# Kernel tuning notes

Hardware: AMD Instinct MI355X
Metric: run time of the kernel (lower is better)

## Reference

```python
import jax, jax.numpy as jnp
import numpy as np

SEASONP = 24
HORIZON = 12
F_WINDOW = 512
N_WINDOWS = 32768


def setup_inputs() -> dict:
    key = jax.random.key(0)
    k1, k2, k3, k4 = jax.random.split(key, 4)
    x = jax.random.uniform(k1, (N_WINDOWS, F_WINDOW), dtype=jnp.float32)
    y = jax.random.uniform(k2, (N_WINDOWS,), dtype=jnp.float32)
    init_L = jax.random.uniform(k3, (N_WINDOWS,), dtype=jnp.float32)
    init_b = jnp.zeros((N_WINDOWS,), dtype=jnp.float32)
    init_S = jax.random.uniform(k4, (N_WINDOWS, SEASONP), dtype=jnp.float32)
    return {
        "x": x,
        "y": y,
        "init_L": init_L,
        "init_b": init_b,
        "init_S": init_S,
        "alpha": jnp.float32(0.3),
        "beta": jnp.float32(0.1),
        "gamma": jnp.float32(0.2),
    }


def reference(x, y, init_L, init_b, init_S, alpha, beta, gamma):
    # Holt-Winters additive-seasonal recurrence, vectorized over N windows.
    # x: [N, F], init_L/init_b: [N], init_S: [N, P]
    N, F = x.shape
    P = init_S.shape[1]
    xt = x.T  # [F, N] time-major for scan
    idxs = jnp.arange(1, F, dtype=jnp.int32)

    def step(carry, inp):
        L, b, S = carry
        xi, i = inp
        si = i % P
        Sv = S[:, si]  # seasonal component for this phase, [N]
        Ln = alpha * (xi - Sv) + (1.0 - alpha) * (L + b)
        bn = beta * (Ln - L) + (1.0 - beta) * b
        Sn = S.at[:, si].set(gamma * (xi - Ln) + (1.0 - gamma) * Sv)
        return (Ln, bn, Sn), None

    (L, b, S), _ = jax.lax.scan(step, (init_L, init_b, init_S), (xt[1:], idxs))

    # forecast: f = (L[-1] + horizon * b[-1]) * S[(i + horizon) % P], i = F-1
    s_idx = (F - 1 + HORIZON) % P
    f = (L + HORIZON * b) * S[:, s_idx]
    loss = jnp.sum((f - y) ** 2)
    return loss
```

## Files before the change

### kernel.cpp

```cpp
#include <hip/hip_runtime.h>


#define F_WINDOW 512
#define SEASONP  24
#define HORIZON  12

#define HW_STEP(xi, si) do {                       \
    const float Sv  = S[si];                       \
    const float d   = (xi) - Sv;                   \
    const float ad  = alpha * d;         \
    const float s_  = L + b;                       \
    const float Ln  = fmaf(oma, s_, ad);           \
    const float abd = beta * ad;         \
    const float tb  = fmaf(omab, b, abd);          \
    const float bn  = fmaf(ab, -L, tb);            \
    const float e   = (xi) - Ln;                   \
    const float gs  = omg * Sv;                    \
    S[si] = fmaf(gamma, e, gs);                    \
    L = Ln; b = bn;                                \
} while (0)

#define HW_BLOCK24(v0, v1, v2, v3, v4, v5) do {                                  \
    HW_STEP(v0.x,  4); HW_STEP(v0.y,  5); HW_STEP(v0.z,  6); HW_STEP(v0.w,  7); \
    HW_STEP(v1.x,  8); HW_STEP(v1.y,  9); HW_STEP(v1.z, 10); HW_STEP(v1.w, 11); \
    HW_STEP(v2.x, 12); HW_STEP(v2.y, 13); HW_STEP(v2.z, 14); HW_STEP(v2.w, 15); \
    HW_STEP(v3.x, 16); HW_STEP(v3.y, 17); HW_STEP(v3.z, 18); HW_STEP(v3.w, 19); \
    HW_STEP(v4.x, 20); HW_STEP(v4.y, 21); HW_STEP(v4.z, 22); HW_STEP(v4.w, 23); \
    HW_STEP(v5.x,  0); HW_STEP(v5.y,  1); HW_STEP(v5.z,  2); HW_STEP(v5.w,  3); \
} while (0)

__global__ __launch_bounds__(64) void holtwinter_kernel(
    const float* __restrict__ x,
    const float* __restrict__ y,
    const float* __restrict__ init_L,
    const float* __restrict__ init_b,
    const float* __restrict__ init_S,
    const float* __restrict__ p_alpha,
    const float* __restrict__ p_beta,
    const float* __restrict__ p_gamma,
    float* __restrict__ out)
{
    const int n = blockIdx.x * 64 + threadIdx.x;

    const float alpha = p_alpha[0];
    const float beta  = p_beta[0];
    const float gamma = p_gamma[0];
    const float oma   = 1.0f - alpha;
    const float ab    = alpha * beta;
    const float omab  = 1.0f - ab;
    const float omg   = 1.0f - gamma;

    const float* __restrict__ xr = x + (size_t)n * F_WINDOW;

    float S[SEASONP];
    {
        const float4* iS4 = (const float4*)(init_S + (size_t)n * SEASONP);
        float4 s0 = iS4[0], s1 = iS4[1], s2 = iS4[2];
        float4 s3 = iS4[3], s4 = iS4[4], s5 = iS4[5];
        S[0]=s0.x;  S[1]=s0.y;  S[2]=s0.z;  S[3]=s0.w;
        S[4]=s1.x;  S[5]=s1.y;  S[6]=s1.z;  S[7]=s1.w;
        S[8]=s2.x;  S[9]=s2.y;  S[10]=s2.z; S[11]=s2.w;
        S[12]=s3.x; S[13]=s3.y; S[14]=s3.z; S[15]=s3.w;
        S[16]=s4.x; S[17]=s4.y; S[18]=s4.z; S[19]=s4.w;
        S[20]=s5.x; S[21]=s5.y; S[22]=s5.z; S[23]=s5.w;
    }

    float L = init_L[n];
    float b = init_b[n];

    {
        const float4 v = *(const float4*)(xr);
        HW_STEP(v.y, 1);
        HW_STEP(v.z, 2);
        HW_STEP(v.w, 3);
    }

    float4 c0, c1, c2, c3, c4, c5;
    {
        const float* __restrict__ xp = xr + 4;
        c0 = *(const float4*)(xp +  0);
        c1 = *(const float4*)(xp +  4);
        c2 = *(const float4*)(xp +  8);
        c3 = *(const float4*)(xp + 12);
        c4 = *(const float4*)(xp + 16);
        c5 = *(const float4*)(xp + 20);
    }
    #pragma unroll 2
    for (int blk = 0; blk < 20; ++blk) {
        const float* __restrict__ np = xr + 4 + (blk + 1) * 24;
        const float4 n0 = *(const float4*)(np +  0);
        const float4 n1 = *(const float4*)(np +  4);
        const float4 n2 = *(const float4*)(np +  8);
        const float4 n3 = *(const float4*)(np + 12);
        const float4 n4 = *(const float4*)(np + 16);
        const float4 n5 = *(const float4*)(np + 20);

        HW_BLOCK24(c0, c1, c2, c3, c4, c5);

        c0 = n0; c1 = n1; c2 = n2; c3 = n3; c4 = n4; c5 = n5;
    }
    HW_BLOCK24(c0, c1, c2, c3, c4, c5);

    {
        const float4 v = *(const float4*)(xr + 508);
        HW_STEP(v.x, 4); HW_STEP(v.y, 5); HW_STEP(v.z, 6); HW_STEP(v.w, 7);
    }

    const float f    = fmaf((float)HORIZON, b, L) * S[19];
    const float diff = f - y[n];
    float val = diff * diff;

    #pragma unroll
    for (int off = 32; off > 0; off >>= 1)
        val += __shfl_down(val, off);
    if (threadIdx.x == 0)
        atomicAdd(out, val);
}

extern "C" void kernel_launch(void* const* d_in, const int* in_sizes, int n_in,
                              void* d_out, int out_size, void* d_ws, size_t ws_size,
                              hipStream_t stream) {
    const float* x      = (const float*)d_in[0];
    const float* y      = (const float*)d_in[1];
    const float* init_L = (const float*)d_in[2];
    const float* init_b = (const float*)d_in[3];
    const float* init_S = (const float*)d_in[4];
    const float* alpha  = (const float*)d_in[5];
    const float* beta   = (const float*)d_in[6];
    const float* gamma  = (const float*)d_in[7];
    float* out = (float*)d_out;

    const int N = in_sizes[1];

    hipMemsetAsync(d_out, 0, sizeof(float), stream);
    holtwinter_kernel<<<N / 64, 64, 0, stream>>>(
        x, y, init_L, init_b, init_S, alpha, beta, gamma, out);
}
```

Measured before the change: 118.7 us.

## Stage x through double-buffered LDS with coalesced cooperative loads

Each thread previously read its own 512-float row with strided float4 loads, so every wavefront load touched 64 separate rows. The new code has the 64-thread block cooperatively load 96-column super-blocks of all 64 rows with coalesced float4 loads into a padded LDS tile (stride 97). The tile is double-buffered so the next super-block's global loads overlap the recurrence on the current one. The final 28 steps still read directly from global memory. This adds about 50 KB of LDS per block, which can limit occupancy, plus scalar LDS reads inside the serial recurrence and 24 float4 staging registers.

```diff
diff --git a/kernel.cpp b/kernel.cpp
--- a/kernel.cpp
+++ b/kernel.cpp
@@ -4,6 +4,9 @@
 #define F_WINDOW 512
 #define SEASONP  24
 #define HORIZON  12
+#define ROWS     64
+#define LSTRIDE  97
+#define SB_F4    24
 
 #define HW_STEP(xi, si) do {                       \
     const float Sv  = S[si];                       \
@@ -20,6 +23,17 @@
     L = Ln; b = bn;                                \
 } while (0)
 
+#define HW_LDS24(row, B) do {                                                                \
+    HW_STEP((row)[(B)+ 0], 4); HW_STEP((row)[(B)+ 1], 5); HW_STEP((row)[(B)+ 2], 6);        \
+    HW_STEP((row)[(B)+ 3], 7); HW_STEP((row)[(B)+ 4], 8); HW_STEP((row)[(B)+ 5], 9);        \
+    HW_STEP((row)[(B)+ 6],10); HW_STEP((row)[(B)+ 7],11); HW_STEP((row)[(B)+ 8],12);        \
+    HW_STEP((row)[(B)+ 9],13); HW_STEP((row)[(B)+10],14); HW_STEP((row)[(B)+11],15);        \
+    HW_STEP((row)[(B)+12],16); HW_STEP((row)[(B)+13],17); HW_STEP((row)[(B)+14],18);        \
+    HW_STEP((row)[(B)+15],19); HW_STEP((row)[(B)+16],20); HW_STEP((row)[(B)+17],21);        \
+    HW_STEP((row)[(B)+18],22); HW_STEP((row)[(B)+19],23); HW_STEP((row)[(B)+20], 0);        \
+    HW_STEP((row)[(B)+21], 1); HW_STEP((row)[(B)+22], 2); HW_STEP((row)[(B)+23], 3);        \
+} while (0)
+
 #define HW_BLOCK24(v0, v1, v2, v3, v4, v5) do {                                  \
     HW_STEP(v0.x,  4); HW_STEP(v0.y,  5); HW_STEP(v0.z,  6); HW_STEP(v0.w,  7); \
     HW_STEP(v1.x,  8); HW_STEP(v1.y,  9); HW_STEP(v1.z, 10); HW_STEP(v1.w, 11); \
@@ -27,6 +41,22 @@
     HW_STEP(v3.x, 16); HW_STEP(v3.y, 17); HW_STEP(v3.z, 18); HW_STEP(v3.w, 19); \
     HW_STEP(v4.x, 20); HW_STEP(v4.y, 21); HW_STEP(v4.z, 22); HW_STEP(v4.w, 23); \
     HW_STEP(v5.x,  0); HW_STEP(v5.y,  1); HW_STEP(v5.z,  2); HW_STEP(v5.w,  3); \
+} while (0)
+
+#define ISSUE_LOADS(sb) do {                                          \
+    const float* gp = xblk + 4 + 96 * (sb);                           \
+    _Pragma("unroll")                                                 \
+    for (int j = 0; j < SB_F4; ++j)                                   \
+        stg[j] = *(const float4*)(gp + goff[j]);                      \
+} while (0)
+
+#define WRITE_LDS(buf) do {                                           \
+    _Pragma("unroll")                                                 \
+    for (int j = 0; j < SB_F4; ++j) {                                 \
+        float* p = (buf) + loff[j];                                   \
+        p[0] = stg[j].x; p[1] = stg[j].y;                             \
+        p[2] = stg[j].z; p[3] = stg[j].w;                             \
+    }                                                                 \
 } while (0)
 
 __global__ __launch_bounds__(64) void holtwinter_kernel(
@@ -40,7 +70,10 @@
     const float* __restrict__ p_gamma,
     float* __restrict__ out)
 {
-    const int n = blockIdx.x * 64 + threadIdx.x;
+    __shared__ float lds[2][ROWS * LSTRIDE];
+
+    const int t = threadIdx.x;
+    const int n = blockIdx.x * ROWS + t;
 
     const float alpha = p_alpha[0];
     const float beta  = p_beta[0];
@@ -50,7 +83,20 @@
     const float omab  = 1.0f - ab;
     const float omg   = 1.0f - gamma;
 
-    const float* __restrict__ xr = x + (size_t)n * F_WINDOW;
+    const float* __restrict__ xblk = x + (size_t)blockIdx.x * ROWS * F_WINDOW;
+    const float* __restrict__ xr   = x + (size_t)n * F_WINDOW;
+
+    int goff[SB_F4], loff[SB_F4];
+    {
+        int r = t / 24, c = t - (t / 24) * 24;
+        #pragma unroll
+        for (int j = 0; j < SB_F4; ++j) {
+            goff[j] = r * F_WINDOW + 4 * c;
+            loff[j] = r * LSTRIDE  + 4 * c;
+            r += 2; c += 16;
+            if (c >= 24) { c -= 24; r += 1; }
+        }
+    }
 
     float S[SEASONP];
     {
@@ -68,6 +114,14 @@
     float L = init_L[n];
     float b = init_b[n];
 
+    float4 stg[SB_F4];
+    float* bcur = lds[0];
+    float* bnxt = lds[1];
+
+    ISSUE_LOADS(0);
+    WRITE_LDS(bcur);
+    __syncthreads();
+
     {
         const float4 v = *(const float4*)(xr);
         HW_STEP(v.y, 1);
@@ -75,35 +129,38 @@
         HW_STEP(v.w, 3);
     }
 
-    float4 c0, c1, c2, c3, c4, c5;
-    {
-        const float* __restrict__ xp = xr + 4;
-        c0 = *(const float4*)(xp +  0);
-        c1 = *(const float4*)(xp +  4);
-        c2 = *(const float4*)(xp +  8);
-        c3 = *(const float4*)(xp + 12);
-        c4 = *(const float4*)(xp + 16);
-        c5 = *(const float4*)(xp + 20);
+    #pragma unroll 1
+    for (int s = 0; s < 4; ++s) {
+        ISSUE_LOADS(s + 1);
+        const float* row = bcur + t * LSTRIDE;
+        HW_LDS24(row,  0);
+        HW_LDS24(row, 24);
+        HW_LDS24(row, 48);
+        HW_LDS24(row, 72);
+        WRITE_LDS(bnxt);
+        __syncthreads();
+        float* tmp = bcur; bcur = bnxt; bnxt = tmp;
     }
-    #pragma unroll 2
-    for (int blk = 0; blk < 20; ++blk) {
-        const float* __restrict__ np = xr + 4 + (blk + 1) * 24;
-        const float4 n0 = *(const float4*)(np +  0);
-        const float4 n1 = *(const float4*)(np +  4);
-        const float4 n2 = *(const float4*)(np +  8);
-        const float4 n3 = *(const float4*)(np + 12);
-        const float4 n4 = *(const float4*)(np + 16);
-        const float4 n5 = *(const float4*)(np + 20);
-
-        HW_BLOCK24(c0, c1, c2, c3, c4, c5);
-
-        c0 = n0; c1 = n1; c2 = n2; c3 = n3; c4 = n4; c5 = n5;
-    }
-    HW_BLOCK24(c0, c1, c2, c3, c4, c5);
 
     {
-        const float4 v = *(const float4*)(xr + 508);
-        HW_STEP(v.x, 4); HW_STEP(v.y, 5); HW_STEP(v.z, 6); HW_STEP(v.w, 7);
+        const float* row = bcur + t * LSTRIDE;
+        HW_LDS24(row,  0);
+        HW_LDS24(row, 24);
+        HW_LDS24(row, 48);
+        HW_LDS24(row, 72);
+    }
+
+    {
+        const float4 v0 = *(const float4*)(xr + 484);
+        const float4 v1 = *(const float4*)(xr + 488);
+        const float4 v2 = *(const float4*)(xr + 492);
+        const float4 v3 = *(const float4*)(xr + 496);
+        const float4 v4 = *(const float4*)(xr + 500);
+        const float4 v5 = *(const float4*)(xr + 504);
+        const float4 v6 = *(const float4*)(xr + 508);
+        HW_BLOCK24(v0, v1, v2, v3, v4, v5);
+        HW_STEP(v6.x, 4); HW_STEP(v6.y, 5);
+        HW_STEP(v6.z, 6); HW_STEP(v6.w, 7);
     }
 
     const float f    = fmaf((float)HORIZON, b, L) * S[19];
@@ -113,7 +170,7 @@
     #pragma unroll
     for (int off = 32; off > 0; off >>= 1)
         val += __shfl_down(val, off);
-    if (threadIdx.x == 0)
+    if (t == 0)
         atomicAdd(out, val);
 }
 
@@ -132,7 +189,7 @@
 
     const int N = in_sizes[1];
 
-    hipMemsetAsync(d_out, 0, sizeof(float), stream);
-    holtwinter_kernel<<<N / 64, 64, 0, stream>>>(
+    hipMemsetAsync(d_out, 0, (size_t)out_size * sizeof(float), stream);
+    holtwinter_kernel<<<N / ROWS, ROWS, 0, stream>>>(
         x, y, init_L, init_b, init_S, alpha, beta, gamma, out);
 }
```

Measured after the change: 137.8 us. 1.16x slower.

## Triple-buffer input rows to prefetch two seasonal blocks ahead

Applied to the files above, without the earlier changes.

Replaces the double-buffered per-block load loop with a three-stage register rotation (A/B/C), so each 24-step block's loads are issued two blocks before they are consumed. The tail vectors, y, init_L and init_b are also loaded up front to hide their latency behind the recurrence. The aim is to hide global memory latency behind the serial dependency chain, since each thread reads its own strided row. In exchange it raises register pressure with 72 live floats of prefetch, which could lower occupancy or cause spills.

```diff
diff --git a/kernel.cpp b/kernel.cpp
--- a/kernel.cpp
+++ b/kernel.cpp
@@ -29,6 +29,15 @@
     HW_STEP(v5.x,  0); HW_STEP(v5.y,  1); HW_STEP(v5.z,  2); HW_STEP(v5.w,  3); \
 } while (0)
 
+#define LOAD6(Bn, base) do {                                \
+    Bn##0 = *(const float4*)((base) +  0);                  \
+    Bn##1 = *(const float4*)((base) +  4);                  \
+    Bn##2 = *(const float4*)((base) +  8);                  \
+    Bn##3 = *(const float4*)((base) + 12);                  \
+    Bn##4 = *(const float4*)((base) + 16);                  \
+    Bn##5 = *(const float4*)((base) + 20);                  \
+} while (0)
+
 __global__ __launch_bounds__(64) void holtwinter_kernel(
     const float* __restrict__ x,
     const float* __restrict__ y,
@@ -52,6 +61,18 @@
 
     const float* __restrict__ xr = x + (size_t)n * F_WINDOW;
 
+    float4 A0, A1, A2, A3, A4, A5;
+    float4 B0, B1, B2, B3, B4, B5;
+    float4 C0, C1, C2, C3, C4, C5;
+
+    LOAD6(A, xr + 4);
+    LOAD6(B, xr + 4 + 24);
+    const float4 P = *(const float4*)(xr);
+    const float4 T = *(const float4*)(xr + 508);
+    const float  yv = y[n];
+    const float  L0 = init_L[n];
+    const float  b0 = init_b[n];
+
     float S[SEASONP];
     {
         const float4* iS4 = (const float4*)(init_S + (size_t)n * SEASONP);
@@ -65,49 +86,32 @@
         S[20]=s5.x; S[21]=s5.y; S[22]=s5.z; S[23]=s5.w;
     }
 
-    float L = init_L[n];
-    float b = init_b[n];
+    float L = L0;
+    float b = b0;
 
-    {
-        const float4 v = *(const float4*)(xr);
-        HW_STEP(v.y, 1);
-        HW_STEP(v.z, 2);
-        HW_STEP(v.w, 3);
+    HW_STEP(P.y, 1);
+    HW_STEP(P.z, 2);
+    HW_STEP(P.w, 3);
+
+    #pragma unroll 1
+    for (int k = 0; k < 6; ++k) {
+        const float* base = xr + 4 + 72 * k;
+        LOAD6(C, base + 48);
+        HW_BLOCK24(A0, A1, A2, A3, A4, A5);
+        LOAD6(A, base + 72);
+        HW_BLOCK24(B0, B1, B2, B3, B4, B5);
+        LOAD6(B, base + 96);
+        HW_BLOCK24(C0, C1, C2, C3, C4, C5);
     }
+    LOAD6(C, xr + 4 + 24 * 20);
+    HW_BLOCK24(A0, A1, A2, A3, A4, A5);
+    HW_BLOCK24(B0, B1, B2, B3, B4, B5);
+    HW_BLOCK24(C0, C1, C2, C3, C4, C5);
 
-    float4 c0, c1, c2, c3, c4, c5;
-    {
-        const float* __restrict__ xp = xr + 4;
-        c0 = *(const float4*)(xp +  0);
-        c1 = *(const float4*)(xp +  4);
-        c2 = *(const float4*)(xp +  8);
-        c3 = *(const float4*)(xp + 12);
-        c4 = *(const float4*)(xp + 16);
-        c5 = *(const float4*)(xp + 20);
-    }
-    #pragma unroll 2
-    for (int blk = 0; blk < 20; ++blk) {
-        const float* __restrict__ np = xr + 4 + (blk + 1) * 24;
-        const float4 n0 = *(const float4*)(np +  0);
-        const float4 n1 = *(const float4*)(np +  4);
-        const float4 n2 = *(const float4*)(np +  8);
-        const float4 n3 = *(const float4*)(np + 12);
-        const float4 n4 = *(const float4*)(np + 16);
-        const float4 n5 = *(const float4*)(np + 20);
-
-        HW_BLOCK24(c0, c1, c2, c3, c4, c5);
-
-        c0 = n0; c1 = n1; c2 = n2; c3 = n3; c4 = n4; c5 = n5;
-    }
-    HW_BLOCK24(c0, c1, c2, c3, c4, c5);
-
-    {
-        const float4 v = *(const float4*)(xr + 508);
-        HW_STEP(v.x, 4); HW_STEP(v.y, 5); HW_STEP(v.z, 6); HW_STEP(v.w, 7);
-    }
+    HW_STEP(T.x, 4); HW_STEP(T.y, 5); HW_STEP(T.z, 6); HW_STEP(T.w, 7);
 
     const float f    = fmaf((float)HORIZON, b, L) * S[19];
-    const float diff = f - y[n];
+    const float diff = f - yv;
     float val = diff * diff;
 
     #pragma unroll
@@ -132,7 +136,7 @@
 
     const int N = in_sizes[1];
 
-    hipMemsetAsync(d_out, 0, sizeof(float), stream);
+    hipMemsetAsync(d_out, 0, (size_t)out_size * sizeof(float), stream);
     holtwinter_kernel<<<N / 64, 64, 0, stream>>>(
         x, y, init_L, init_b, init_S, alpha, beta, gamma, out);
 }
```

After: 121.5 us. 2.4% more time.
